# Kernel optimization log

Measured on AMD Instinct MI355X. Metric: run time of the kernel, lower is better.

## Reference

```python
import jax, jax.numpy as jnp
import numpy as np


def dct_matrices(N):
    # torch_dct-style unnormalized DCT-II (norm=None): X_k = 2 * sum_n x_n cos(pi*(2n+1)k/(2N))
    n = jnp.arange(N, dtype=jnp.float32)
    ang = jnp.pi * (2.0 * n[None, :] + 1.0) * n[:, None] / (2.0 * N)  # [k, n]
    D = 2.0 * jnp.cos(ang)                                            # forward DCT matrix [k, n]
    w = jnp.where(n == 0, 0.5, 1.0)                                   # half-weight on DC term
    M = (jnp.cos(ang).T * w[None, :]) / (2.0 * N)                     # inverse DCT matrix [n, k]
    return D, M


def setup_inputs() -> dict:
    key = jax.random.key(0)
    k1, k2, k3 = jax.random.split(key, 3)
    B, c_in, c_out, H, W, kh, kw = 8, 64, 128, 128, 128, 5, 5
    K = float(np.sqrt(1.0 / (c_in * kh * kw)))
    x = jax.random.normal(k1, (B, c_in, H, W), dtype=jnp.float32)
    weight = (2.0 * jax.random.uniform(k2, (c_out, c_in, kh, kw), dtype=jnp.float32) - 1.0) * K
    bias = (2.0 * jax.random.uniform(k3, (c_out,), dtype=jnp.float32) - 1.0) * K
    return {"x": x, "weight": weight, "bias": bias}


def reference(x, weight, bias):
    B, c_in, H, W = x.shape
    c_out, _, kh, kw = weight.shape
    D, M = dct_matrices(H)

    # DCT-II along H axis of input
    xd = jnp.einsum('kh,bchw->bckw', D, x)            # (B, c_in, H, W)
    xf = jnp.fft.rfft(xd, axis=-1)                    # (B, c_in, H, Wf) complex

    # Pad kernel along H to full size, DCT along H, rFFT along W with n=W
    wpad = jnp.pad(weight, ((0, 0), (0, 0), (0, H - kh), (0, 0)))
    wd = jnp.einsum('kh,oihw->oikw', D, wpad)         # (c_out, c_in, H, kw)
    wf = jnp.fft.rfft(wd, n=W, axis=-1)               # (c_out, c_in, H, Wf) complex

    # Broadcast complex multiply + reduce over c_in (fused via einsum)
    hf = jnp.einsum('bchw,ochw->bohw', xf, wf)        # (B, c_out, H, Wf)
    h = jnp.fft.irfft(hf, n=W, axis=-1)               # (B, c_out, H, W)

    # Inverse DCT along H, add bias, stride slice (stride = 1)
    h = jnp.einsum('nk,bokw->bonw', M, h) + bias[None, :, None, None]
    return h[:, :, ::1, ::1]
```

## Files before the change

### kernel.cpp

```cpp
#include <hip/hip_runtime.h>


using half8v = __attribute__((ext_vector_type(8))) _Float16;
using half4v = __attribute__((ext_vector_type(4))) _Float16;
using f32x4  = __attribute__((ext_vector_type(4))) float;

#define PI_F 3.14159265358979323846f

__device__ __forceinline__ int sw_off(int n, int k, int K, int mask) {
    int c = k >> 3;
    return n * K + (((c ^ (n & mask)) << 3) | (k & 7));
}

__global__ void k_dm(_Float16* __restrict__ D, _Float16* __restrict__ M) {
    int k = blockIdx.x;
    int h = threadIdx.x;
    float ang = PI_F * (float)((2 * h + 1) * k) * (1.0f / 256.0f);
    float c = cosf(ang);
    D[k * 128 + h] = (_Float16)(2.0f * c);
    float wk = (k == 0) ? 0.5f : 1.0f;
    M[h * 128 + k] = (_Float16)(c * wk * (1.0f / 256.0f));
}

__global__ __launch_bounds__(256) void k_wd(const float* __restrict__ w, _Float16* __restrict__ WD) {
    __shared__ float lw[1600];
    __shared__ float lcos[320];
    int co = blockIdx.x >> 1, k0 = (blockIdx.x & 1) << 6;
    int tid = threadIdx.x;

    for (int e = tid; e < 1600; e += 256) lw[e] = w[co * 1600 + e];
    for (int e = tid; e < 320; e += 256) {
        int kl = e / 5, i = e - kl * 5;
        lcos[e] = 2.0f * cosf(PI_F * (float)((2 * i + 1) * (k0 + kl)) * (1.0f / 256.0f));
    }
    __syncthreads();

    for (int e = tid; e < 20480; e += 256) {
        int kk = e & 31, rest = e >> 5;
        int s = rest % 10, kl = rest / 10;
        int j = s >> 1, ci = ((s & 1) << 5) + kk;
        const float* wp = &lw[ci * 25 + j];
        const float* cp = &lcos[kl * 5];
        float acc = 0.f;
#pragma unroll
        for (int i = 0; i < 5; ++i) acc += cp[i] * wp[i * 5];
        WD[(((long)(k0 + kl) * 10 + s) * 128 + co) * 32 + kk] = (_Float16)acc;
    }
}

__device__ __forceinline__ void gemm128_gA(const _Float16* __restrict__ gA,
                                           const _Float16* lB,
                                           f32x4 acc[4][4], int tid) {
    int lane = tid & 63, ln = lane & 15, q = lane >> 4;
    int wave = tid >> 6, wm = wave >> 1, wn = wave & 1;
#pragma unroll
    for (int s = 0; s < 4; ++s) {
        half8v af[4], bf[4];
#pragma unroll
        for (int mt = 0; mt < 4; ++mt) {
            int m = wm * 64 + mt * 16 + ln;
            af[mt] = *(const half8v*)(&gA[m * 128 + (s * 4 + q) * 8]);
        }
#pragma unroll
        for (int nt = 0; nt < 4; ++nt) {
            int n = wn * 64 + nt * 16 + ln;
            bf[nt] = *(const half8v*)(&lB[n * 128 + (((s * 4 + q) ^ (n & 15)) << 3)]);
        }
#pragma unroll
        for (int mt = 0; mt < 4; ++mt)
#pragma unroll
            for (int nt = 0; nt < 4; ++nt)
                acc[mt][nt] = __builtin_amdgcn_mfma_f32_16x16x32_f16(af[mt], bf[nt], acc[mt][nt], 0, 0, 0);
    }
}

__device__ __forceinline__ void stage_transB(const _Float16* __restrict__ src, int row_stride,
                                             _Float16* l, int K, int mask, int nblocks, int tid) {
    for (int blk = tid; blk < nblocks; blk += 256) {
        int kb = blk >> 4, wb = blk & 15;
        int k0 = kb * 4, w0 = wb * 8;
        half8v r0 = *(const half8v*)(&src[(k0 + 0) * row_stride + w0]);
        half8v r1 = *(const half8v*)(&src[(k0 + 1) * row_stride + w0]);
        half8v r2 = *(const half8v*)(&src[(k0 + 2) * row_stride + w0]);
        half8v r3 = *(const half8v*)(&src[(k0 + 3) * row_stride + w0]);
#pragma unroll
        for (int dw = 0; dw < 8; ++dw) {
            int n = w0 + dw;
            half4v p = {r0[dw], r1[dw], r2[dw], r3[dw]};
            *(half4v*)(&l[sw_off(n, k0, K, mask)]) = p;
        }
    }
}

__global__ __launch_bounds__(256) void k_dctH(const float* __restrict__ x,
                                              const _Float16* __restrict__ Dg,
                                              _Float16* __restrict__ xd) {
    __shared__ _Float16 lB[128 * 128];
    int b = blockIdx.x >> 6, ci = blockIdx.x & 63;
    int tid = threadIdx.x;

    const float* xs = x + (long)(b * 64 + ci) * 16384;
#pragma unroll
    for (int rep = 0; rep < 2; ++rep) {
        int blk = tid + rep * 256;
        int hb = blk >> 4, wb = blk & 15;
        int h0 = hb * 4, w0 = wb * 8;
        f32x4 f[4][2];
#pragma unroll
        for (int dh = 0; dh < 4; ++dh) {
            f[dh][0] = *(const f32x4*)(&xs[(h0 + dh) * 128 + w0]);
            f[dh][1] = *(const f32x4*)(&xs[(h0 + dh) * 128 + w0 + 4]);
        }
#pragma unroll
        for (int dw = 0; dw < 8; ++dw) {
            int n = w0 + dw;
            half4v p = {(_Float16)f[0][dw >> 2][dw & 3], (_Float16)f[1][dw >> 2][dw & 3],
                        (_Float16)f[2][dw >> 2][dw & 3], (_Float16)f[3][dw >> 2][dw & 3]};
            *(half4v*)(&lB[sw_off(n, h0, 128, 15)]) = p;
        }
    }
    __syncthreads();

    f32x4 acc[4][4] = {};
    gemm128_gA(Dg, lB, acc, tid);

    int lane = tid & 63, ln = lane & 15, q = lane >> 4;
    int wave = tid >> 6, wm = wave >> 1, wn = wave & 1;
#pragma unroll
    for (int mt = 0; mt < 4; ++mt)
#pragma unroll
        for (int nt = 0; nt < 4; ++nt)
#pragma unroll
            for (int r = 0; r < 4; ++r) {
                int kk = wm * 64 + mt * 16 + q * 4 + r;
                int wcol = wn * 64 + nt * 16 + ln;
                xd[((long)(kk * 8 + b) * 64 + ci) * 128 + wcol] = (_Float16)acc[mt][nt][r];
            }
}

__global__ __launch_bounds__(256) void k_conv(const _Float16* __restrict__ xd,
                                              const _Float16* __restrict__ WD,
                                              _Float16* __restrict__ y2) {
    __shared__ _Float16 lX[128 * 64];
    int bid = blockIdx.x;
    int k = bid & 127, b = bid >> 7;
    int tid = threadIdx.x;

    const _Float16* xs = xd + (long)(k * 8 + b) * 8192;
    stage_transB(xs, 128, lX, 64, 7, 256, tid);
    __syncthreads();

    int lane = tid & 63, ln = lane & 15, q = lane >> 4;
    int wave = tid >> 6, wm = wave >> 1, wn = wave & 1;
    f32x4 acc[4][4] = {};

    const _Float16* wkb = WD + (long)k * 40960;

    for (int s = 0; s < 10; ++s) {
        int j = s >> 1;
        int cb = (s & 1) << 2;
        const _Float16* wt = wkb + s * 4096;
        half8v af[4], bf[4];
#pragma unroll
        for (int mt = 0; mt < 4; ++mt) {
            int m = wm * 64 + mt * 16 + ln;
            af[mt] = *(const half8v*)(&wt[m * 32 + q * 8]);
        }
#pragma unroll
        for (int nt = 0; nt < 4; ++nt) {
            int wcol = wn * 64 + nt * 16 + ln;
            int n = (wcol - j) & 127;
            bf[nt] = *(const half8v*)(&lX[n * 64 + (((cb + q) ^ (n & 7)) << 3)]);
        }
#pragma unroll
        for (int mt = 0; mt < 4; ++mt)
#pragma unroll
            for (int nt = 0; nt < 4; ++nt)
                acc[mt][nt] = __builtin_amdgcn_mfma_f32_16x16x32_f16(af[mt], bf[nt], acc[mt][nt], 0, 0, 0);
    }

    _Float16* yb = y2 + (long)(b * 128 + k) * 16384;
#pragma unroll
    for (int mt = 0; mt < 4; ++mt)
#pragma unroll
        for (int nt = 0; nt < 4; ++nt)
#pragma unroll
            for (int r = 0; r < 4; ++r) {
                int co = wm * 64 + mt * 16 + q * 4 + r;
                int wcol = wn * 64 + nt * 16 + ln;
                yb[co * 128 + wcol] = (_Float16)acc[mt][nt][r];
            }
}

__global__ __launch_bounds__(256) void k_idct(const _Float16* __restrict__ y2,
                                              const _Float16* __restrict__ Mg,
                                              const float* __restrict__ bias,
                                              float* __restrict__ out) {
    __shared__ _Float16 lB[128 * 128];
    int b = blockIdx.x >> 7, co = blockIdx.x & 127;
    int tid = threadIdx.x;

    const _Float16* src = y2 + (long)b * 2097152 + co * 128;
    stage_transB(src, 16384, lB, 128, 15, 512, tid);
    __syncthreads();

    f32x4 acc[4][4] = {};
    gemm128_gA(Mg, lB, acc, tid);

    float bv = bias[co];
    float* ob = out + ((long)(b * 128 + co)) * 16384;
    int lane = tid & 63, ln = lane & 15, q = lane >> 4;
    int wave = tid >> 6, wm = wave >> 1, wn = wave & 1;
#pragma unroll
    for (int mt = 0; mt < 4; ++mt)
#pragma unroll
        for (int nt = 0; nt < 4; ++nt)
#pragma unroll
            for (int r = 0; r < 4; ++r) {
                int h = wm * 64 + mt * 16 + q * 4 + r;
                int wcol = wn * 64 + nt * 16 + ln;
                ob[h * 128 + wcol] = acc[mt][nt][r] + bv;
            }
}

extern "C" void kernel_launch(void* const* d_in, const int* in_sizes, int n_in,
                              void* d_out, int out_size, void* d_ws, size_t ws_size,
                              hipStream_t stream) {
    const float* x    = (const float*)d_in[0];
    const float* w    = (const float*)d_in[1];
    const float* bias = (const float*)d_in[2];
    float* out = (float*)d_out;

    char* ws = (char*)d_ws;
    _Float16* D  = (_Float16*)(ws);
    _Float16* M  = (_Float16*)(ws + 32768);
    _Float16* WD = (_Float16*)(ws + 65536);
    _Float16* xd = (_Float16*)(ws + 65536 + 10485760);
    _Float16* y2 = (_Float16*)(ws + 65536 + 10485760 + 16777216);

    k_dm  <<<dim3(128),  dim3(128), 0, stream>>>(D, M);
    k_wd  <<<dim3(256),  dim3(256), 0, stream>>>(w, WD);
    k_dctH<<<dim3(512),  dim3(256), 0, stream>>>(x, D, xd);
    k_conv<<<dim3(1024), dim3(256), 0, stream>>>(xd, WD, y2);
    k_idct<<<dim3(1024), dim3(256), 0, stream>>>(y2, M, bias, out);
}
```

Before: 149.4 us.

## Swap MFMA operands for vectorized row stores and merge DCT-matrix setup into k_wd

Swaps the A/B operands of the MFMA calls so each lane holds four consecutive output columns. The epilogues of dctH, conv and idct can then write half4/float4 vectors instead of scattered scalar stores. It also folds the D/M matrix generation into the weight-transform kernel to drop one launch, and unrolls the LDS staging loops into fixed-size variants. Correctness depends on the transposed accumulator layout matching the new index mapping.

```diff
diff --git a/kernel.cpp b/kernel.cpp
--- a/kernel.cpp
+++ b/kernel.cpp
@@ -12,21 +12,24 @@
     return n * K + (((c ^ (n & mask)) << 3) | (k & 7));
 }
 
-__global__ void k_dm(_Float16* __restrict__ D, _Float16* __restrict__ M) {
-    int k = blockIdx.x;
-    int h = threadIdx.x;
-    float ang = PI_F * (float)((2 * h + 1) * k) * (1.0f / 256.0f);
-    float c = cosf(ang);
-    D[k * 128 + h] = (_Float16)(2.0f * c);
-    float wk = (k == 0) ? 0.5f : 1.0f;
-    M[h * 128 + k] = (_Float16)(c * wk * (1.0f / 256.0f));
-}
-
-__global__ __launch_bounds__(256) void k_wd(const float* __restrict__ w, _Float16* __restrict__ WD) {
+__global__ __launch_bounds__(256) void k_wd(const float* __restrict__ w,
+                                            _Float16* __restrict__ WD,
+                                            _Float16* __restrict__ D,
+                                            _Float16* __restrict__ M) {
     __shared__ float lw[1600];
     __shared__ float lcos[320];
-    int co = blockIdx.x >> 1, k0 = (blockIdx.x & 1) << 6;
-    int tid = threadIdx.x;
+    int bid = blockIdx.x;
+    int co = bid >> 1, k0 = (bid & 1) << 6;
+    int tid = threadIdx.x;
+
+    if (bid < 128 && tid < 128) {
+        int k = bid, h = tid;
+        float ang = PI_F * (float)((2 * h + 1) * k) * (1.0f / 256.0f);
+        float c = cosf(ang);
+        D[k * 128 + h] = (_Float16)(2.0f * c);
+        float wk = (k == 0) ? 0.5f : 1.0f;
+        M[h * 128 + k] = (_Float16)(c * wk * (1.0f / 256.0f));
+    }
 
     for (int e = tid; e < 1600; e += 256) lw[e] = w[co * 1600 + e];
     for (int e = tid; e < 320; e += 256) {
@@ -48,9 +51,9 @@
     }
 }
 
-__device__ __forceinline__ void gemm128_gA(const _Float16* __restrict__ gA,
-                                           const _Float16* lB,
-                                           f32x4 acc[4][4], int tid) {
+__device__ __forceinline__ void gemm128_gA_T(const _Float16* __restrict__ gA,
+                                             const _Float16* lB,
+                                             f32x4 acc[4][4], int tid) {
     int lane = tid & 63, ln = lane & 15, q = lane >> 4;
     int wave = tid >> 6, wm = wave >> 1, wn = wave & 1;
 #pragma unroll
@@ -70,25 +73,48 @@
         for (int mt = 0; mt < 4; ++mt)
 #pragma unroll
             for (int nt = 0; nt < 4; ++nt)
-                acc[mt][nt] = __builtin_amdgcn_mfma_f32_16x16x32_f16(af[mt], bf[nt], acc[mt][nt], 0, 0, 0);
-    }
-}
-
-__device__ __forceinline__ void stage_transB(const _Float16* __restrict__ src, int row_stride,
-                                             _Float16* l, int K, int mask, int nblocks, int tid) {
-    for (int blk = tid; blk < nblocks; blk += 256) {
-        int kb = blk >> 4, wb = blk & 15;
-        int k0 = kb * 4, w0 = wb * 8;
-        half8v r0 = *(const half8v*)(&src[(k0 + 0) * row_stride + w0]);
-        half8v r1 = *(const half8v*)(&src[(k0 + 1) * row_stride + w0]);
-        half8v r2 = *(const half8v*)(&src[(k0 + 2) * row_stride + w0]);
-        half8v r3 = *(const half8v*)(&src[(k0 + 3) * row_stride + w0]);
-#pragma unroll
-        for (int dw = 0; dw < 8; ++dw) {
-            int n = w0 + dw;
-            half4v p = {r0[dw], r1[dw], r2[dw], r3[dw]};
-            *(half4v*)(&l[sw_off(n, k0, K, mask)]) = p;
-        }
+                acc[mt][nt] = __builtin_amdgcn_mfma_f32_16x16x32_f16(bf[nt], af[mt], acc[mt][nt], 0, 0, 0);
+    }
+}
+
+__device__ __forceinline__ void stage_transB64(const _Float16* __restrict__ src, int row_stride,
+                                               _Float16* l, int tid) {
+    int kb = tid >> 4, wb = tid & 15;
+    int k0 = kb * 4, w0 = wb * 8;
+    half8v r0 = *(const half8v*)(&src[(k0 + 0) * row_stride + w0]);
+    half8v r1 = *(const half8v*)(&src[(k0 + 1) * row_stride + w0]);
+    half8v r2 = *(const half8v*)(&src[(k0 + 2) * row_stride + w0]);
+    half8v r3 = *(const half8v*)(&src[(k0 + 3) * row_stride + w0]);
+#pragma unroll
+    for (int dw = 0; dw < 8; ++dw) {
+        int n = w0 + dw;
+        half4v p = {r0[dw], r1[dw], r2[dw], r3[dw]};
+        *(half4v*)(&l[sw_off(n, k0, 64, 7)]) = p;
+    }
+}
+
+__device__ __forceinline__ void stage_transB128(const _Float16* __restrict__ src, int row_stride,
+                                                _Float16* l, int tid) {
+    int blkA = tid, blkB = tid + 256;
+    int kA = (blkA >> 4) * 4, wA = (blkA & 15) * 8;
+    int kB = (blkB >> 4) * 4, wB = (blkB & 15) * 8;
+    half8v a0 = *(const half8v*)(&src[(kA + 0) * row_stride + wA]);
+    half8v a1 = *(const half8v*)(&src[(kA + 1) * row_stride + wA]);
+    half8v a2 = *(const half8v*)(&src[(kA + 2) * row_stride + wA]);
+    half8v a3 = *(const half8v*)(&src[(kA + 3) * row_stride + wA]);
+    half8v b0 = *(const half8v*)(&src[(kB + 0) * row_stride + wB]);
+    half8v b1 = *(const half8v*)(&src[(kB + 1) * row_stride + wB]);
+    half8v b2 = *(const half8v*)(&src[(kB + 2) * row_stride + wB]);
+    half8v b3 = *(const half8v*)(&src[(kB + 3) * row_stride + wB]);
+#pragma unroll
+    for (int dw = 0; dw < 8; ++dw) {
+        half4v p = {a0[dw], a1[dw], a2[dw], a3[dw]};
+        *(half4v*)(&l[sw_off(wA + dw, kA, 128, 15)]) = p;
+    }
+#pragma unroll
+    for (int dw = 0; dw < 8; ++dw) {
+        half4v p = {b0[dw], b1[dw], b2[dw], b3[dw]};
+        *(half4v*)(&l[sw_off(wB + dw, kB, 128, 15)]) = p;
     }
 }
 
@@ -122,20 +148,20 @@
     __syncthreads();
 
     f32x4 acc[4][4] = {};
-    gemm128_gA(Dg, lB, acc, tid);
+    gemm128_gA_T(Dg, lB, acc, tid);
 
     int lane = tid & 63, ln = lane & 15, q = lane >> 4;
     int wave = tid >> 6, wm = wave >> 1, wn = wave & 1;
 #pragma unroll
     for (int mt = 0; mt < 4; ++mt)
 #pragma unroll
-        for (int nt = 0; nt < 4; ++nt)
-#pragma unroll
-            for (int r = 0; r < 4; ++r) {
-                int kk = wm * 64 + mt * 16 + q * 4 + r;
-                int wcol = wn * 64 + nt * 16 + ln;
-                xd[((long)(kk * 8 + b) * 64 + ci) * 128 + wcol] = (_Float16)acc[mt][nt][r];
-            }
+        for (int nt = 0; nt < 4; ++nt) {
+            int kk = wm * 64 + mt * 16 + ln;
+            int w0 = wn * 64 + nt * 16 + q * 4;
+            half4v p = {(_Float16)acc[mt][nt][0], (_Float16)acc[mt][nt][1],
+                        (_Float16)acc[mt][nt][2], (_Float16)acc[mt][nt][3]};
+            *(half4v*)(&xd[((long)(kk * 8 + b) * 64 + ci) * 128 + w0]) = p;
+        }
 }
 
 __global__ __launch_bounds__(256) void k_conv(const _Float16* __restrict__ xd,
@@ -147,7 +173,7 @@
     int tid = threadIdx.x;
 
     const _Float16* xs = xd + (long)(k * 8 + b) * 8192;
-    stage_transB(xs, 128, lX, 64, 7, 256, tid);
+    stage_transB64(xs, 128, lX, tid);
     __syncthreads();
 
     int lane = tid & 63, ln = lane & 15, q = lane >> 4;
@@ -176,20 +202,20 @@
         for (int mt = 0; mt < 4; ++mt)
 #pragma unroll
             for (int nt = 0; nt < 4; ++nt)
-                acc[mt][nt] = __builtin_amdgcn_mfma_f32_16x16x32_f16(af[mt], bf[nt], acc[mt][nt], 0, 0, 0);
+                acc[mt][nt] = __builtin_amdgcn_mfma_f32_16x16x32_f16(bf[nt], af[mt], acc[mt][nt], 0, 0, 0);
     }
 
     _Float16* yb = y2 + (long)(b * 128 + k) * 16384;
 #pragma unroll
     for (int mt = 0; mt < 4; ++mt)
 #pragma unroll
-        for (int nt = 0; nt < 4; ++nt)
-#pragma unroll
-            for (int r = 0; r < 4; ++r) {
-                int co = wm * 64 + mt * 16 + q * 4 + r;
-                int wcol = wn * 64 + nt * 16 + ln;
-                yb[co * 128 + wcol] = (_Float16)acc[mt][nt][r];
-            }
+        for (int nt = 0; nt < 4; ++nt) {
+            int co = wm * 64 + mt * 16 + ln;
+            int w0 = wn * 64 + nt * 16 + q * 4;
+            half4v p = {(_Float16)acc[mt][nt][0], (_Float16)acc[mt][nt][1],
+                        (_Float16)acc[mt][nt][2], (_Float16)acc[mt][nt][3]};
+            *(half4v*)(&yb[co * 128 + w0]) = p;
+        }
 }
 
 __global__ __launch_bounds__(256) void k_idct(const _Float16* __restrict__ y2,
@@ -201,11 +227,11 @@
     int tid = threadIdx.x;
 
     const _Float16* src = y2 + (long)b * 2097152 + co * 128;
-    stage_transB(src, 16384, lB, 128, 15, 512, tid);
+    stage_transB128(src, 16384, lB, tid);
     __syncthreads();
 
     f32x4 acc[4][4] = {};
-    gemm128_gA(Mg, lB, acc, tid);
+    gemm128_gA_T(Mg, lB, acc, tid);
 
     float bv = bias[co];
     float* ob = out + ((long)(b * 128 + co)) * 16384;
@@ -214,13 +240,13 @@
 #pragma unroll
     for (int mt = 0; mt < 4; ++mt)
 #pragma unroll
-        for (int nt = 0; nt < 4; ++nt)
-#pragma unroll
-            for (int r = 0; r < 4; ++r) {
-                int h = wm * 64 + mt * 16 + q * 4 + r;
-                int wcol = wn * 64 + nt * 16 + ln;
-                ob[h * 128 + wcol] = acc[mt][nt][r] + bv;
-            }
+        for (int nt = 0; nt < 4; ++nt) {
+            int h = wm * 64 + mt * 16 + ln;
+            int w0 = wn * 64 + nt * 16 + q * 4;
+            f32x4 p = {acc[mt][nt][0] + bv, acc[mt][nt][1] + bv,
+                       acc[mt][nt][2] + bv, acc[mt][nt][3] + bv};
+            *(f32x4*)(&ob[h * 128 + w0]) = p;
+        }
 }
 
 extern "C" void kernel_launch(void* const* d_in, const int* in_sizes, int n_in,
@@ -238,8 +264,7 @@
     _Float16* xd = (_Float16*)(ws + 65536 + 10485760);
     _Float16* y2 = (_Float16*)(ws + 65536 + 10485760 + 16777216);
 
-    k_dm  <<<dim3(128),  dim3(128), 0, stream>>>(D, M);
-    k_wd  <<<dim3(256),  dim3(256), 0, stream>>>(w, WD);
+    k_wd  <<<dim3(256),  dim3(256), 0, stream>>>(w, WD, D, M);
     k_dctH<<<dim3(512),  dim3(256), 0, stream>>>(x, D, xd);
     k_conv<<<dim3(1024), dim3(256), 0, stream>>>(xd, WD, y2);
     k_idct<<<dim3(1024), dim3(256), 0, stream>>>(y2, M, bias, out);
```

New measurement: 150.2 us. About the same (+0.6%).
